# Kernel tuning notes

Measured on AMD Instinct MI355X. Metric: run time of the kernel, lower is better.

The kernel has to match this reference:

```python
import jax, jax.numpy as jnp
import numpy as np


def setup_inputs() -> dict:
    key = jax.random.key(0)
    k1, k2 = jax.random.split(key)
    n, c, H, W = 8, 16, 512, 512
    pred = jax.random.normal(k1, (n, c, H, W), dtype=jnp.float32)
    target = jax.random.randint(k2, (n, H, W), 0, c, dtype=jnp.int64)
    weights = jnp.ones((n, 1, H, W), dtype=jnp.float32)  # ignored by the module
    return {"pred": pred, "target": target, "weights": weights}


def reference(pred, target, weights):
    # pred: [n,c,H,W] logits; target: [n,H,W] int class ids; weights arg is ignored
    n, c, H, W = pred.shape
    # Global (whole-batch) per-class pixel counts -> inverse-frequency weights.
    counts = jnp.zeros((c,), dtype=pred.dtype).at[target.reshape(-1)].add(1.0)
    w_class = jnp.where(counts > 0, 1.0 / (counts * c), 0.0)  # [c]
    w = w_class[target]  # [n,H,W] per-pixel weight (constant w.r.t. pred)
    # log-softmax gathered at target class per pixel
    logp = jax.nn.log_softmax(pred, axis=1)  # [n,c,H,W]
    lp_t = jnp.take_along_axis(logp, target[:, None, :, :], axis=1)[:, 0]  # [n,H,W]
    num = (lp_t * w).reshape(n, -1).sum(axis=1)  # [n]
    den = w.reshape(n, -1).sum(axis=1)           # [n]
    return -(num / den).mean()
```

## Files before the change

### kernel.cpp

```cpp
#include <hip/hip_runtime.h>

#define NIMG 8
#define NCLS 16
#define HW   262144
#define NBLK 2048

__global__ __launch_bounds__(256) void dwce_main(const float* __restrict__ pred,
                                                 const int* __restrict__ tgt,
                                                 float* __restrict__ partials) {
    __shared__ float s_bin[32];
    const int tid = threadIdx.x;
    if (tid < 32) s_bin[tid] = 0.0f;
    __syncthreads();

    const int gid = blockIdx.x * 256 + tid;
    const long long p0 = (long long)gid * 4;
    const int n_img = (int)(p0 >> 18);
    const int hw    = (int)(p0 & (HW - 1));
    const float* base = pred + (size_t)n_img * NCLS * HW + hw;

    const int4 t = *(const int4*)(tgt + p0);

    float4 v[2][4];
#pragma unroll
    for (int j = 0; j < 4; ++j)
        v[0][j] = *(const float4*)(base + (size_t)j * HW);

    float4 m  = make_float4(-3.0e38f, -3.0e38f, -3.0e38f, -3.0e38f);
    float4 s  = make_float4(0.f, 0.f, 0.f, 0.f);
    float4 xt = make_float4(0.f, 0.f, 0.f, 0.f);

#pragma unroll
    for (int chunk = 0; chunk < 4; ++chunk) {
        const int cur = chunk & 1;
        if (chunk < 3) {
#pragma unroll
            for (int j = 0; j < 4; ++j)
                v[cur ^ 1][j] = *(const float4*)(base + (size_t)((chunk + 1) * 4 + j) * HW);
        }
        float4 mc = v[cur][0];
#pragma unroll
        for (int j = 1; j < 4; ++j) {
            mc.x = fmaxf(mc.x, v[cur][j].x);
            mc.y = fmaxf(mc.y, v[cur][j].y);
            mc.z = fmaxf(mc.z, v[cur][j].z);
            mc.w = fmaxf(mc.w, v[cur][j].w);
        }
        float4 mn;
        mn.x = fmaxf(m.x, mc.x);
        mn.y = fmaxf(m.y, mc.y);
        mn.z = fmaxf(m.z, mc.z);
        mn.w = fmaxf(m.w, mc.w);
        s.x *= __expf(m.x - mn.x);
        s.y *= __expf(m.y - mn.y);
        s.z *= __expf(m.z - mn.z);
        s.w *= __expf(m.w - mn.w);
#pragma unroll
        for (int j = 0; j < 4; ++j) {
            const int c = chunk * 4 + j;
            const float4 vv = v[cur][j];
            s.x += __expf(vv.x - mn.x);
            s.y += __expf(vv.y - mn.y);
            s.z += __expf(vv.z - mn.z);
            s.w += __expf(vv.w - mn.w);
            if (t.x == c) xt.x = vv.x;
            if (t.y == c) xt.y = vv.y;
            if (t.z == c) xt.z = vv.z;
            if (t.w == c) xt.w = vv.w;
        }
        m = mn;
    }

    const float lp0 = xt.x - (m.x + __logf(s.x));
    const float lp1 = xt.y - (m.y + __logf(s.y));
    const float lp2 = xt.z - (m.z + __logf(s.z));
    const float lp3 = xt.w - (m.w + __logf(s.w));

    atomicAdd(&s_bin[t.x], lp0);
    atomicAdd(&s_bin[t.y], lp1);
    atomicAdd(&s_bin[t.z], lp2);
    atomicAdd(&s_bin[t.w], lp3);
    atomicAdd(&s_bin[16 + t.x], 1.0f);
    atomicAdd(&s_bin[16 + t.y], 1.0f);
    atomicAdd(&s_bin[16 + t.z], 1.0f);
    atomicAdd(&s_bin[16 + t.w], 1.0f);

    __syncthreads();
    if (tid < 32)
        partials[(size_t)tid * NBLK + blockIdx.x] = s_bin[tid];
}

__global__ __launch_bounds__(256) void dwce_final(const float* __restrict__ ws,
                                                  float* __restrict__ out) {
    __shared__ float tot[32][NIMG];
    __shared__ float wcl[NCLS];
    __shared__ float ratio[NIMG];
    const int tid = threadIdx.x;
    const int c = tid >> 3;
    const int n = tid & 7;

    const float4* p = (const float4*)(ws + (size_t)c * NBLK + n * 256);
    float4 a = make_float4(0.f, 0.f, 0.f, 0.f);
#pragma unroll 8
    for (int k = 0; k < 64; ++k) {
        float4 q = p[k];
        a.x += q.x; a.y += q.y; a.z += q.z; a.w += q.w;
    }
    tot[c][n] = (a.x + a.y) + (a.z + a.w);
    __syncthreads();

    if (tid < NCLS) {
        float g = 0.f;
#pragma unroll
        for (int i = 0; i < NIMG; ++i) g += tot[NCLS + tid][i];
        wcl[tid] = (g > 0.f) ? 1.0f / (g * (float)NCLS) : 0.0f;
    }
    __syncthreads();
    if (tid < NIMG) {
        float num = 0.f, den = 0.f;
#pragma unroll
        for (int c2 = 0; c2 < NCLS; ++c2) {
            num += tot[c2][tid] * wcl[c2];
            den += tot[NCLS + c2][tid] * wcl[c2];
        }
        ratio[tid] = num / den;
    }
    __syncthreads();
    if (tid == 0) {
        float r = 0.f;
#pragma unroll
        for (int i = 0; i < NIMG; ++i) r += ratio[i];
        out[0] = -r * (1.0f / (float)NIMG);
    }
}

extern "C" void kernel_launch(void* const* d_in, const int* in_sizes, int n_in,
                              void* d_out, int out_size, void* d_ws, size_t ws_size,
                              hipStream_t stream) {
    const float* pred = (const float*)d_in[0];
    const int*   tgt  = (const int*)d_in[1];
    float* out = (float*)d_out;
    float* ws  = (float*)d_ws;

    dwce_main<<<NBLK, 256, 0, stream>>>(pred, tgt, ws);
    dwce_final<<<1, 256, 0, stream>>>(ws, out);
}
```

Before: 208.8 us.

## Process two pixel groups per thread with streaming online softmax over classes

Halves the block count so each thread handles two float4 pixel groups (8 pixels), and replaces the chunked double-buffered class loop with a per-class online softmax update, unrolled by two. The goal is more independent loads in flight per thread and less launch and partial-reduction overhead, since the final kernel now reduces 1024 partials. The per-class online update adds more exp calls (two per element instead of roughly 1.25), which could make the kernel compute-bound. Fewer blocks also gives lower wave-level parallelism.

Result: slower. 223.0 us (+6.8%).

```diff
diff --git a/kernel.cpp b/kernel.cpp
--- a/kernel.cpp
+++ b/kernel.cpp
@@ -2,8 +2,10 @@
 
 #define NIMG 8
 #define NCLS 16
-#define HW   262144
-#define NBLK 2048
+#define HW      262144
+#define PXB     2048
+#define NBLK    1024
+#define GROUPS  2
 
 __global__ __launch_bounds__(256) void dwce_main(const float* __restrict__ pred,
                                                  const int* __restrict__ tgt,
@@ -13,81 +15,74 @@
     if (tid < 32) s_bin[tid] = 0.0f;
     __syncthreads();
 
-    const int gid = blockIdx.x * 256 + tid;
-    const long long p0 = (long long)gid * 4;
-    const int n_img = (int)(p0 >> 18);
-    const int hw    = (int)(p0 & (HW - 1));
-    const float* base = pred + (size_t)n_img * NCLS * HW + hw;
+    const int b = blockIdx.x;
+    const long long px0 = (long long)b * PXB;
+    const int n_img = (int)(px0 >> 18);
+    const int hw0   = (int)(px0 & (HW - 1));
+    const float* base = pred + (size_t)n_img * NCLS * HW + hw0;
 
-    const int4 t = *(const int4*)(tgt + p0);
+    const int w    = tid >> 6;
+    const int lane = tid & 63;
+    int idx[GROUPS];
+#pragma unroll
+    for (int g = 0; g < GROUPS; ++g)
+        idx[g] = w * (GROUPS * 256) + g * 256 + lane * 4;
 
-    float4 v[2][4];
+    int4 t[GROUPS];
 #pragma unroll
-    for (int j = 0; j < 4; ++j)
-        v[0][j] = *(const float4*)(base + (size_t)j * HW);
+    for (int g = 0; g < GROUPS; ++g)
+        t[g] = *(const int4*)(tgt + px0 + idx[g]);
 
-    float4 m  = make_float4(-3.0e38f, -3.0e38f, -3.0e38f, -3.0e38f);
-    float4 s  = make_float4(0.f, 0.f, 0.f, 0.f);
-    float4 xt = make_float4(0.f, 0.f, 0.f, 0.f);
+    float4 m[GROUPS], s[GROUPS], xt[GROUPS];
+#pragma unroll
+    for (int g = 0; g < GROUPS; ++g) {
+        m[g]  = make_float4(-3.0e38f, -3.0e38f, -3.0e38f, -3.0e38f);
+        s[g]  = make_float4(0.f, 0.f, 0.f, 0.f);
+        xt[g] = make_float4(0.f, 0.f, 0.f, 0.f);
+    }
+
+#pragma unroll 2
+    for (int c = 0; c < NCLS; ++c) {
+        const float* cb = base + (size_t)c * HW;
+#pragma unroll
+        for (int g = 0; g < GROUPS; ++g) {
+            const float4 v = *(const float4*)(cb + idx[g]);
+            float4 mn;
+            mn.x = fmaxf(m[g].x, v.x);
+            mn.y = fmaxf(m[g].y, v.y);
+            mn.z = fmaxf(m[g].z, v.z);
+            mn.w = fmaxf(m[g].w, v.w);
+            s[g].x = s[g].x * __expf(m[g].x - mn.x) + __expf(v.x - mn.x);
+            s[g].y = s[g].y * __expf(m[g].y - mn.y) + __expf(v.y - mn.y);
+            s[g].z = s[g].z * __expf(m[g].z - mn.z) + __expf(v.z - mn.z);
+            s[g].w = s[g].w * __expf(m[g].w - mn.w) + __expf(v.w - mn.w);
+            m[g] = mn;
+            if (t[g].x == c) xt[g].x = v.x;
+            if (t[g].y == c) xt[g].y = v.y;
+            if (t[g].z == c) xt[g].z = v.z;
+            if (t[g].w == c) xt[g].w = v.w;
+        }
+    }
 
 #pragma unroll
-    for (int chunk = 0; chunk < 4; ++chunk) {
-        const int cur = chunk & 1;
-        if (chunk < 3) {
-#pragma unroll
-            for (int j = 0; j < 4; ++j)
-                v[cur ^ 1][j] = *(const float4*)(base + (size_t)((chunk + 1) * 4 + j) * HW);
-        }
-        float4 mc = v[cur][0];
-#pragma unroll
-        for (int j = 1; j < 4; ++j) {
-            mc.x = fmaxf(mc.x, v[cur][j].x);
-            mc.y = fmaxf(mc.y, v[cur][j].y);
-            mc.z = fmaxf(mc.z, v[cur][j].z);
-            mc.w = fmaxf(mc.w, v[cur][j].w);
-        }
-        float4 mn;
-        mn.x = fmaxf(m.x, mc.x);
-        mn.y = fmaxf(m.y, mc.y);
-        mn.z = fmaxf(m.z, mc.z);
-        mn.w = fmaxf(m.w, mc.w);
-        s.x *= __expf(m.x - mn.x);
-        s.y *= __expf(m.y - mn.y);
-        s.z *= __expf(m.z - mn.z);
-        s.w *= __expf(m.w - mn.w);
-#pragma unroll
-        for (int j = 0; j < 4; ++j) {
-            const int c = chunk * 4 + j;
-            const float4 vv = v[cur][j];
-            s.x += __expf(vv.x - mn.x);
-            s.y += __expf(vv.y - mn.y);
-            s.z += __expf(vv.z - mn.z);
-            s.w += __expf(vv.w - mn.w);
-            if (t.x == c) xt.x = vv.x;
-            if (t.y == c) xt.y = vv.y;
-            if (t.z == c) xt.z = vv.z;
-            if (t.w == c) xt.w = vv.w;
-        }
-        m = mn;
+    for (int g = 0; g < GROUPS; ++g) {
+        const float lp0 = xt[g].x - (m[g].x + __logf(s[g].x));
+        const float lp1 = xt[g].y - (m[g].y + __logf(s[g].y));
+        const float lp2 = xt[g].z - (m[g].z + __logf(s[g].z));
+        const float lp3 = xt[g].w - (m[g].w + __logf(s[g].w));
+        atomicAdd(&s_bin[t[g].x], lp0);
+        atomicAdd(&s_bin[t[g].y], lp1);
+        atomicAdd(&s_bin[t[g].z], lp2);
+        atomicAdd(&s_bin[t[g].w], lp3);
+        atomicAdd(&s_bin[16 + t[g].x], 1.0f);
+        atomicAdd(&s_bin[16 + t[g].y], 1.0f);
+        atomicAdd(&s_bin[16 + t[g].z], 1.0f);
+        atomicAdd(&s_bin[16 + t[g].w], 1.0f);
     }
-
-    const float lp0 = xt.x - (m.x + __logf(s.x));
-    const float lp1 = xt.y - (m.y + __logf(s.y));
-    const float lp2 = xt.z - (m.z + __logf(s.z));
-    const float lp3 = xt.w - (m.w + __logf(s.w));
-
-    atomicAdd(&s_bin[t.x], lp0);
-    atomicAdd(&s_bin[t.y], lp1);
-    atomicAdd(&s_bin[t.z], lp2);
-    atomicAdd(&s_bin[t.w], lp3);
-    atomicAdd(&s_bin[16 + t.x], 1.0f);
-    atomicAdd(&s_bin[16 + t.y], 1.0f);
-    atomicAdd(&s_bin[16 + t.z], 1.0f);
-    atomicAdd(&s_bin[16 + t.w], 1.0f);
 
     __syncthreads();
     if (tid < 32)
-        partials[(size_t)tid * NBLK + blockIdx.x] = s_bin[tid];
+        partials[(size_t)tid * NBLK + b] = s_bin[tid];
 }
 
 __global__ __launch_bounds__(256) void dwce_final(const float* __restrict__ ws,
@@ -99,10 +94,10 @@
     const int c = tid >> 3;
     const int n = tid & 7;
 
-    const float4* p = (const float4*)(ws + (size_t)c * NBLK + n * 256);
+    const float4* p = (const float4*)(ws + (size_t)c * NBLK + n * 128);
     float4 a = make_float4(0.f, 0.f, 0.f, 0.f);
 #pragma unroll 8
-    for (int k = 0; k < 64; ++k) {
+    for (int k = 0; k < 32; ++k) {
         float4 q = p[k];
         a.x += q.x; a.y += q.y; a.z += q.z; a.w += q.w;
     }
```
